# Kernel tuning notes

Measured on AMD Instinct MI355X. Metric: run time of the kernel, lower is better.

## Reference

```python
import jax, jax.numpy as jnp
import numpy as np

N, E, G = 20000, 320000, 64
IN_CH, HID, HEADS = 128, 64, 8
LEAKY_SLOPE = 0.2
SOFTMAX_EPS = 1e-16


def setup_inputs() -> dict:
    key = jax.random.key(0)
    ks = jax.random.split(key, 12)
    s = lambda fan_in: 1.0 / np.sqrt(fan_in)
    return {
        "x": jax.random.normal(ks[0], (N, IN_CH), jnp.float32),
        "edge_index": jax.random.randint(ks[1], (2, E), 0, N, jnp.int32),
        "batch": jnp.sort(jax.random.randint(ks[2], (N,), 0, G, jnp.int32)),
        "W1": jax.random.normal(ks[3], (HEADS * HID, IN_CH), jnp.float32) * s(IN_CH),
        "att_src1": jax.random.normal(ks[4], (HEADS, HID), jnp.float32) * s(HID),
        "att_dst1": jax.random.normal(ks[5], (HEADS, HID), jnp.float32) * s(HID),
        "b1": jnp.zeros((HEADS * HID,), jnp.float32),
        "W2": jax.random.normal(ks[6], (HID, HEADS * HID), jnp.float32) * s(HEADS * HID),
        "att_src2": jax.random.normal(ks[7], (1, HID), jnp.float32) * s(HID),
        "att_dst2": jax.random.normal(ks[8], (1, HID), jnp.float32) * s(HID),
        "b2": jnp.zeros((HID,), jnp.float32),
    }


def gat_conv(x, src, dst, W, att_src, att_dst, b):
    # x: [N, F_in]; W: [H*C, F_in]; att_*: [H, C]; b: [H*C]
    n = x.shape[0]
    heads, ch = att_src.shape
    h = (x @ W.T).reshape(n, heads, ch)                    # [N,H,C]
    a_s = jnp.einsum('nhc,hc->nh', h, att_src)             # [N,H]
    a_d = jnp.einsum('nhc,hc->nh', h, att_dst)             # [N,H]
    e = jax.nn.leaky_relu(a_s[src] + a_d[dst], LEAKY_SLOPE)  # [E,H]
    m = jax.ops.segment_max(e, dst, num_segments=n)        # scatter-softmax (stable)
    e = jnp.exp(e - m[dst])
    z = jax.ops.segment_sum(e, dst, num_segments=n)
    alpha = e / (z[dst] + SOFTMAX_EPS)                     # [E,H]
    msg = h[src] * alpha[:, :, None]                       # [E,H,C]
    out = jax.ops.segment_sum(msg, dst, num_segments=n)    # [N,H,C]
    return out.reshape(n, heads * ch) + b


def reference(x, edge_index, batch, W1, att_src1, att_dst1, b1, W2, att_src2, att_dst2, b2):
    # PyG GATConv default: add self loops
    loop = jnp.arange(N, dtype=edge_index.dtype)
    src = jnp.concatenate([edge_index[0], loop])
    dst = jnp.concatenate([edge_index[1], loop])

    x_mid = jax.nn.relu(gat_conv(x, src, dst, W1, att_src1, att_dst1, b1))  # [N, H*C]

    # global_mean_pool over `batch` segments
    sums = jax.ops.segment_sum(x_mid, batch, num_segments=G)
    cnt = jax.ops.segment_sum(jnp.ones((N,), x_mid.dtype), batch, num_segments=G)
    gat_mid_pooled = sums / jnp.maximum(cnt, 1.0)[:, None]                  # [G, H*C]

    # dropout identity in eval mode
    x_late = gat_conv(x_mid, src, dst, W2, att_src2, att_dst2, b2)          # [N, C]
    gat_late_view = x_late.reshape(-1, HEADS * HID)                          # [N/H, H*C]
    return gat_mid_pooled, gat_late_view
```

## Files before the change

### kernel.cpp

```cpp
#include <hip/hip_runtime.h>
#include <math.h>

#define NN 20000
#define EE 320000
#define ETOT 340000
#define GG 64
#define INCH 128
#define HIDC 64
#define NH 8
#define HC 512
#define SLOPE 0.2f
#define SMEPS 1e-16f

typedef unsigned short u16;
typedef unsigned int u32;
typedef __attribute__((ext_vector_type(8))) short bf16x8;
typedef __attribute__((ext_vector_type(4))) float f32x4;
typedef __attribute__((ext_vector_type(2))) float f32x2;
typedef __attribute__((ext_vector_type(2))) u32 u32x2;

__device__ __forceinline__ float rlanef(float v, int l) {
  return __uint_as_float(__builtin_amdgcn_readlane(__float_as_uint(v), l));
}
__device__ __forceinline__ u16 f2bf(float f) {
  u32 x = __float_as_uint(f);
  x += 0x7FFFu + ((x >> 16) & 1u);
  return (u16)(x >> 16);
}
__device__ __forceinline__ float bflo(u32 w) { return __uint_as_float(w << 16); }
__device__ __forceinline__ float bfhi(u32 w) { return __uint_as_float(w & 0xffff0000u); }

__global__ void k_hist(const int* __restrict__ ei, int* __restrict__ deg) {
  int i = blockIdx.x * 256 + threadIdx.x;
  if (i >= ETOT) return;
  int d = (i < EE) ? ei[EE + i] : (i - EE);
  atomicAdd(&deg[d], 1);
}

__global__ void k_scan(const int* __restrict__ deg, int* __restrict__ rowstart) {
  __shared__ int wsum[16];
  __shared__ int carry_sh;
  int tid = threadIdx.x;
  int lane = tid & 63, w = tid >> 6;
  if (tid == 0) { carry_sh = 0; rowstart[0] = 0; }
  __syncthreads();
  for (int base = 0; base < NN; base += 1024) {
    int v = (base + tid < NN) ? deg[base + tid] : 0;
    int s = v;
#pragma unroll
    for (int off = 1; off < 64; off <<= 1) {
      int t = __shfl_up(s, off);
      if (lane >= off) s += t;
    }
    if (lane == 63) wsum[w] = s;
    __syncthreads();
    if (w == 0 && lane < 16) {
      int t = wsum[lane];
#pragma unroll
      for (int off = 1; off < 16; off <<= 1) {
        int u = __shfl_up(t, off);
        if (lane >= off) t += u;
      }
      wsum[lane] = t;
    }
    __syncthreads();
    int waveoff = (w == 0) ? 0 : wsum[w - 1];
    int incl = s + waveoff + carry_sh;
    if (base + tid < NN) rowstart[base + tid + 1] = incl;
    __syncthreads();
    if (tid == 1023) carry_sh = incl;
    __syncthreads();
  }
}

__global__ void k_fill(const int* __restrict__ ei, const int* __restrict__ rowstart,
                       int* __restrict__ wcur, int* __restrict__ csr) {
  int i = blockIdx.x * 256 + threadIdx.x;
  if (i >= ETOT) return;
  int s, d;
  if (i < EE) { s = ei[i]; d = ei[EE + i]; } else { s = i - EE; d = s; }
  int pos = rowstart[d] + atomicAdd(&wcur[d], 1);
  csr[pos] = s;
}

__global__ void k_prep(const float* __restrict__ W1, const float* __restrict__ W2,
                       const float* __restrict__ as1, const float* __restrict__ ad1v,
                       const float* __restrict__ x,
                       u16* __restrict__ W1bf, u16* __restrict__ W2bf,
                       float* __restrict__ wB1, u16* __restrict__ xbf) {
  int i = blockIdx.x * 256 + threadIdx.x;
  if (i < 65536) {
    W1bf[i] = f2bf(W1[i]);
  } else if (i < 65536 + 32768) {
    int j = i - 65536;
    W2bf[j] = f2bf(W2[j]);
  } else if (i < 65536 + 32768 + 2048) {
    int j = i - 65536 - 32768;
    int k = j >> 4, c = j & 15;
    int h = c & 7;
    const float* av = (c < 8) ? as1 : ad1v;
    float s = 0.f;
    for (int q = 0; q < 64; ++q) s += W1[(h * 64 + q) * 128 + k] * av[h * 64 + q];
    wB1[j] = s;
  } else {
    int j = i - 100352;
    if (j < NN * INCH) xbf[j] = f2bf(x[j]);
  }
}

__global__ __launch_bounds__(256) void k_logits1(
    const float* __restrict__ x, const float* __restrict__ wB1,
    float* __restrict__ al1) {
  __shared__ float bs[128][16];
  int tid = threadIdx.x;
#pragma unroll
  for (int i = 0; i < 8; ++i) {
    int e = tid + i * 256;
    bs[e >> 4][e & 15] = wB1[e];
  }
  __syncthreads();
  int gt = blockIdx.x * 256 + tid;
  int r = gt >> 2; if (r > NN - 1) r = NN - 1;
  int q = gt & 3;
  const float* xp = x + (size_t)r * INCH;
  float acc[4] = {0.f, 0.f, 0.f, 0.f};
  for (int kq = 0; kq < 32; ++kq) {
    float4 a = *(const float4*)(xp + kq * 4);
    float av[4] = {a.x, a.y, a.z, a.w};
#pragma unroll
    for (int kk = 0; kk < 4; ++kk) {
      const float4 b = *(const float4*)&bs[kq * 4 + kk][q * 4];
      acc[0] = fmaf(av[kk], b.x, acc[0]);
      acc[1] = fmaf(av[kk], b.y, acc[1]);
      acc[2] = fmaf(av[kk], b.z, acc[2]);
      acc[3] = fmaf(av[kk], b.w, acc[3]);
    }
  }
  float4 o; o.x = acc[0]; o.y = acc[1]; o.z = acc[2]; o.w = acc[3];
  *(float4*)(al1 + (size_t)r * 16 + q * 4) = o;
}

__global__ __launch_bounds__(256) void k_agg1(
    const u16* __restrict__ xbf, const float* __restrict__ al1,
    const int* __restrict__ rowstart, const int* __restrict__ csr,
    u16* __restrict__ aggbf) {
  int n = blockIdx.x * 4 + (threadIdx.x >> 6);
  int lane = threadIdx.x & 63;
  int rs = __builtin_amdgcn_readfirstlane(rowstart[n]);
  int re = __builtin_amdgcn_readfirstlane(rowstart[n + 1]);
  float4 ad0 = *(const float4*)(al1 + (size_t)n * 16 + 8);
  float4 ad1 = *(const float4*)(al1 + (size_t)n * 16 + 12);
  float zp[NH] = {};
  f32x2 acc2[NH] = {};
  for (int base = rs; base < re; base += 64) {
    int cn = min(64, re - base);
    int idx = base + ((lane < cn) ? lane : 0);
    int s = csr[idx];
    float4 a0 = *(const float4*)(al1 + (size_t)s * 16);
    float4 a1 = *(const float4*)(al1 + (size_t)s * 16 + 4);
    float e[8] = {a0.x + ad0.x, a0.y + ad0.y, a0.z + ad0.z, a0.w + ad0.w,
                  a1.x + ad1.x, a1.y + ad1.y, a1.z + ad1.z, a1.w + ad1.w};
    float p[8];
#pragma unroll
    for (int h = 0; h < 8; ++h) {
      float t = e[h];
      t = fmaxf(t, SLOPE * t);
      float pv = __expf(t);
      pv = (lane < cn) ? pv : 0.f;
      p[h] = pv;
      zp[h] += pv;
    }
    int j = 0;
    for (; j + 1 < cn; j += 2) {
      int sa = __builtin_amdgcn_readlane(s, j);
      int sb = __builtin_amdgcn_readlane(s, j + 1);
      u32 xa = *(const u32*)(xbf + (size_t)sa * INCH + lane * 2);
      u32 xb = *(const u32*)(xbf + (size_t)sb * INCH + lane * 2);
      f32x2 va; va.x = bflo(xa); va.y = bfhi(xa);
      f32x2 vb; vb.x = bflo(xb); vb.y = bfhi(xb);
#pragma unroll
      for (int h = 0; h < 8; ++h) {
        float pa = rlanef(p[h], j);
        float pb = rlanef(p[h], j + 1);
        f32x2 pa2; pa2.x = pa; pa2.y = pa;
        f32x2 pb2; pb2.x = pb; pb2.y = pb;
        acc2[h] = __builtin_elementwise_fma(pa2, va, acc2[h]);
        acc2[h] = __builtin_elementwise_fma(pb2, vb, acc2[h]);
      }
    }
    if (j < cn) {
      int sa = __builtin_amdgcn_readlane(s, j);
      u32 xa = *(const u32*)(xbf + (size_t)sa * INCH + lane * 2);
      f32x2 va; va.x = bflo(xa); va.y = bfhi(xa);
#pragma unroll
      for (int h = 0; h < 8; ++h) {
        float pa = rlanef(p[h], j);
        f32x2 pa2; pa2.x = pa; pa2.y = pa;
        acc2[h] = __builtin_elementwise_fma(pa2, va, acc2[h]);
      }
    }
  }
#pragma unroll
  for (int h = 0; h < 8; ++h) {
    float z = zp[h];
#pragma unroll
    for (int off = 32; off; off >>= 1) z += __shfl_xor(z, off);
    float inv = 1.f / (z + SMEPS);
    u32 pk = ((u32)f2bf(acc2[h].y * inv) << 16) | (u32)f2bf(acc2[h].x * inv);
    *(u32*)(aggbf + (size_t)h * NN * INCH + (size_t)n * INCH + lane * 2) = pk;
  }
}

__global__ __launch_bounds__(256) void k_gemm1h(
    const u16* __restrict__ aggbf, const u16* __restrict__ W1bf,
    const float* __restrict__ b1, u16* __restrict__ xmidbf) {
  int tid = threadIdx.x;
  int head = blockIdx.x & 7;
  int nb = blockIdx.x >> 3;
  int w = tid >> 6, l = tid & 63;
  int li = l & 15, hi = l >> 4;
  const u16* Ab = aggbf + (size_t)head * NN * INCH;
  const u16* Bb = W1bf + (size_t)head * 64 * INCH;

  bf16x8 Bf[4][4];
#pragma unroll
  for (int ks = 0; ks < 4; ++ks)
#pragma unroll
    for (int ct = 0; ct < 4; ++ct)
      Bf[ks][ct] = *(const bf16x8*)(Bb + (size_t)(ct * 16 + li) * INCH + ks * 32 + hi * 8);

  int nA = nb * 64 + w * 16 + li; if (nA > NN - 1) nA = NN - 1;
  const u16* Ap = Ab + (size_t)nA * INCH + hi * 8;
  f32x4 acc[4] = {};
#pragma unroll
  for (int ks = 0; ks < 4; ++ks) {
    bf16x8 Af = *(const bf16x8*)(Ap + ks * 32);
#pragma unroll
    for (int ct = 0; ct < 4; ++ct)
      acc[ct] = __builtin_amdgcn_mfma_f32_16x16x32_bf16(Af, Bf[ks][ct], acc[ct], 0, 0, 0);
  }
#pragma unroll
  for (int ct = 0; ct < 4; ++ct) {
    float bb = b1[head * 64 + ct * 16 + li];
#pragma unroll
    for (int reg = 0; reg < 4; ++reg) {
      int r = nb * 64 + w * 16 + hi * 4 + reg; if (r > NN - 1) r = NN - 1;
      float v = fmaxf(acc[ct][reg] + bb, 0.f);
      xmidbf[(size_t)r * HC + head * 64 + ct * 16 + li] = f2bf(v);
    }
  }
}

__global__ __launch_bounds__(256) void k_gemm2(
    const u16* __restrict__ xmb, const u16* __restrict__ W2bf,
    const float* __restrict__ atts, const float* __restrict__ attd,
    u16* __restrict__ h2bf, float* __restrict__ as2, float* __restrict__ ad2) {
  __shared__ float red[4][16][65];
  int tid = threadIdx.x;
  int w = tid >> 6, l = tid & 63;
  int li = l & 15, hi = l >> 4;
  int brow = blockIdx.x * 16;

  bf16x8 Bf[4][4];
#pragma unroll
  for (int ksl = 0; ksl < 4; ++ksl)
#pragma unroll
    for (int ct = 0; ct < 4; ++ct)
      Bf[ksl][ct] = *(const bf16x8*)(W2bf + (size_t)(ct * 16 + li) * HC + w * 128 + ksl * 32 + hi * 8);

  const u16* Ap = xmb + (size_t)(brow + li) * HC + w * 128 + hi * 8;
  f32x4 acc[4] = {};
#pragma unroll
  for (int ksl = 0; ksl < 4; ++ksl) {
    bf16x8 Af = *(const bf16x8*)(Ap + ksl * 32);
#pragma unroll
    for (int ct = 0; ct < 4; ++ct)
      acc[ct] = __builtin_amdgcn_mfma_f32_16x16x32_bf16(Af, Bf[ksl][ct], acc[ct], 0, 0, 0);
  }
#pragma unroll
  for (int ct = 0; ct < 4; ++ct)
#pragma unroll
    for (int reg = 0; reg < 4; ++reg)
      red[w][hi * 4 + reg][ct * 16 + li] = acc[ct][reg];
  __syncthreads();

  int c = l;
  float atv = atts[c], adv = attd[c];
  float vs[4], vd[4];
#pragma unroll
  for (int i = 0; i < 4; ++i) {
    int r = w + 4 * i;
    float v = red[0][r][c] + red[1][r][c] + red[2][r][c] + red[3][r][c];
    h2bf[(size_t)(brow + r) * HIDC + c] = f2bf(v);
    vs[i] = v * atv; vd[i] = v * adv;
  }
#pragma unroll
  for (int off = 32; off; off >>= 1) {
#pragma unroll
    for (int i = 0; i < 4; ++i) { vs[i] += __shfl_xor(vs[i], off); vd[i] += __shfl_xor(vd[i], off); }
  }
  if (l == 0) {
#pragma unroll
    for (int i = 0; i < 4; ++i) {
      int n = brow + w + 4 * i;
      as2[n] = vs[i]; ad2[n] = vd[i];
    }
  }
}

__global__ __launch_bounds__(256) void k_node2(
    const u16* __restrict__ h2bf, const float* __restrict__ as2, const float* __restrict__ ad2,
    const int* __restrict__ rowstart, const int* __restrict__ csr,
    const float* __restrict__ b2, float* __restrict__ out) {
  int n = blockIdx.x * 4 + (threadIdx.x >> 6);
  int lane = threadIdx.x & 63;
  int e = lane >> 4, c = lane & 15;
  int rs = __builtin_amdgcn_readfirstlane(rowstart[n]);
  int re = __builtin_amdgcn_readfirstlane(rowstart[n + 1]);
  float ad = ad2[n];
  f32x2 accA = {}, accB = {};
  float zp = 0.f;
  for (int base = rs; base < re; base += 4) {
    int idx = base + e;
    bool ok = idx < re;
    int s = csr[ok ? idx : re - 1];
    float t = as2[s] + ad;
    t = fmaxf(t, SLOPE * t);
    float pv = __expf(t);
    float p = ok ? pv : 0.f;
    zp += p;
    const u32* hp = (const u32*)(h2bf + (size_t)s * HIDC + c * 4);
    u32 w0 = hp[0], w1 = hp[1];
    f32x2 v0; v0.x = bflo(w0); v0.y = bfhi(w0);
    f32x2 v1; v1.x = bflo(w1); v1.y = bfhi(w1);
    f32x2 p2; p2.x = p; p2.y = p;
    accA = __builtin_elementwise_fma(p2, v0, accA);
    accB = __builtin_elementwise_fma(p2, v1, accB);
  }
  float acc0 = accA.x, acc1 = accA.y, acc2v = accB.x, acc3 = accB.y;
  zp += __shfl_xor(zp, 16); zp += __shfl_xor(zp, 32);
  acc0 += __shfl_xor(acc0, 16); acc0 += __shfl_xor(acc0, 32);
  acc1 += __shfl_xor(acc1, 16); acc1 += __shfl_xor(acc1, 32);
  acc2v += __shfl_xor(acc2v, 16); acc2v += __shfl_xor(acc2v, 32);
  acc3 += __shfl_xor(acc3, 16); acc3 += __shfl_xor(acc3, 32);
  if (e == 0) {
    float inv = 1.f / (zp + SMEPS);
    float4 bv = *(const float4*)(b2 + c * 4);
    float4 o;
    o.x = acc0 * inv + bv.x; o.y = acc1 * inv + bv.y;
    o.z = acc2v * inv + bv.z; o.w = acc3 * inv + bv.w;
    *(float4*)(out + (size_t)n * HIDC + c * 4) = o;
  }
}

__device__ inline int lowerb(const int* a, int n, int v) {
  int lo = 0, hi = n;
  while (lo < hi) { int mid = (lo + hi) >> 1; if (a[mid] < v) lo = mid + 1; else hi = mid; }
  return lo;
}

__global__ __launch_bounds__(256) void k_pool(const u16* __restrict__ xmb,
                                              const int* __restrict__ batch,
                                              float* __restrict__ out) {
  __shared__ float red[4][128];
  int g = blockIdx.x >> 2;
  int cb = blockIdx.x & 3;
  int tid = threadIdx.x;
  int c2 = tid & 63;
  int rq = tid >> 6;
  int lo = lowerb(batch, NN, g);
  int hi = lowerb(batch, NN, g + 1);
  float sx = 0.f, sy = 0.f;
  for (int n = lo + rq; n < hi; n += 4) {
    u32 w = *(const u32*)(xmb + (size_t)n * HC + cb * 128 + c2 * 2);
    sx += bflo(w); sy += bfhi(w);
  }
  red[rq][c2 * 2] = sx; red[rq][c2 * 2 + 1] = sy;
  __syncthreads();
  if (rq == 0) {
    float inv = 1.f / fmaxf((float)(hi - lo), 1.f);
    float vx = red[0][c2 * 2] + red[1][c2 * 2] + red[2][c2 * 2] + red[3][c2 * 2];
    float vy = red[0][c2 * 2 + 1] + red[1][c2 * 2 + 1] + red[2][c2 * 2 + 1] + red[3][c2 * 2 + 1];
    float2 o; o.x = vx * inv; o.y = vy * inv;
    *(float2*)(out + (size_t)g * HC + cb * 128 + c2 * 2) = o;
  }
}

extern "C" void kernel_launch(void* const* d_in, const int* in_sizes, int n_in,
                              void* d_out, int out_size, void* d_ws, size_t ws_size,
                              hipStream_t stream) {
  const float* x     = (const float*)d_in[0];
  const int*   ei    = (const int*)d_in[1];
  const int*   batch = (const int*)d_in[2];
  const float* W1    = (const float*)d_in[3];
  const float* atts1 = (const float*)d_in[4];
  const float* attd1 = (const float*)d_in[5];
  const float* b1    = (const float*)d_in[6];
  const float* W2    = (const float*)d_in[7];
  const float* atts2 = (const float*)d_in[8];
  const float* attd2 = (const float*)d_in[9];
  const float* b2    = (const float*)d_in[10];
  float* out = (float*)d_out;

  float* ws = (float*)d_ws;
  size_t off = 0;
  u16*  aggbf  = (u16*)(ws + off); off += (size_t)NH * NN * INCH / 2;
  u16*  xmidbf = (u16*)(ws + off); off += (size_t)NN * HC / 2;
  u16*  h2bf   = (u16*)(ws + off); off += (size_t)NN * HIDC / 2;
  float* al1  = ws + off; off += (size_t)NN * 16;
  float* as2  = ws + off; off += NN;
  float* ad2  = ws + off; off += NN;
  u16*  W1bf  = (u16*)(ws + off); off += 65536 / 2;
  u16*  W2bf  = (u16*)(ws + off); off += 32768 / 2;
  float* wB1  = ws + off; off += 2048;
  u16*  xbf   = (u16*)(ws + off); off += (size_t)NN * INCH / 2;
  int* deg      = (int*)(ws + off); off += NN;
  int* wcur     = (int*)(ws + off); off += NN;
  int* rowstart = (int*)(ws + off); off += NN + 4;
  int* csr      = (int*)(ws + off); off += ETOT;

  hipMemsetAsync(deg, 0, sizeof(int) * 2 * NN, stream);
  k_prep<<<10392, 256, 0, stream>>>(W1, W2, atts1, attd1, x, W1bf, W2bf, wB1, xbf);
  k_hist<<<(ETOT + 255) / 256, 256, 0, stream>>>(ei, deg);
  k_scan<<<1, 1024, 0, stream>>>(deg, rowstart);
  k_fill<<<(ETOT + 255) / 256, 256, 0, stream>>>(ei, rowstart, wcur, csr);

  k_logits1<<<313, 256, 0, stream>>>(x, wB1, al1);
  k_agg1<<<5000, 256, 0, stream>>>(xbf, al1, rowstart, csr, aggbf);
  k_gemm1h<<<313 * 8, 256, 0, stream>>>(aggbf, W1bf, b1, xmidbf);
  k_pool<<<GG * 4, 256, 0, stream>>>(xmidbf, batch, out);
  k_gemm2<<<1250, 256, 0, stream>>>(xmidbf, W2bf, atts2, attd2, h2bf, as2, ad2);
  k_node2<<<5000, 256, 0, stream>>>(h2bf, as2, ad2, rowstart, csr, b2, out + (size_t)GG * HC);
}
```

Measured before the change: 200.2 us.

## Fuse histogram into prep, single-pass scan, deeper unroll in aggregation loops

```diff
diff --git a/kernel.cpp b/kernel.cpp
--- a/kernel.cpp
+++ b/kernel.cpp
@@ -17,7 +17,6 @@
 typedef __attribute__((ext_vector_type(8))) short bf16x8;
 typedef __attribute__((ext_vector_type(4))) float f32x4;
 typedef __attribute__((ext_vector_type(2))) float f32x2;
-typedef __attribute__((ext_vector_type(2))) u32 u32x2;
 
 __device__ __forceinline__ float rlanef(float v, int l) {
   return __uint_as_float(__builtin_amdgcn_readlane(__float_as_uint(v), l));
@@ -30,64 +29,22 @@
 __device__ __forceinline__ float bflo(u32 w) { return __uint_as_float(w << 16); }
 __device__ __forceinline__ float bfhi(u32 w) { return __uint_as_float(w & 0xffff0000u); }
 
-__global__ void k_hist(const int* __restrict__ ei, int* __restrict__ deg) {
-  int i = blockIdx.x * 256 + threadIdx.x;
-  if (i >= ETOT) return;
-  int d = (i < EE) ? ei[EE + i] : (i - EE);
-  atomicAdd(&deg[d], 1);
-}
-
-__global__ void k_scan(const int* __restrict__ deg, int* __restrict__ rowstart) {
-  __shared__ int wsum[16];
-  __shared__ int carry_sh;
-  int tid = threadIdx.x;
-  int lane = tid & 63, w = tid >> 6;
-  if (tid == 0) { carry_sh = 0; rowstart[0] = 0; }
-  __syncthreads();
-  for (int base = 0; base < NN; base += 1024) {
-    int v = (base + tid < NN) ? deg[base + tid] : 0;
-    int s = v;
-#pragma unroll
-    for (int off = 1; off < 64; off <<= 1) {
-      int t = __shfl_up(s, off);
-      if (lane >= off) s += t;
-    }
-    if (lane == 63) wsum[w] = s;
-    __syncthreads();
-    if (w == 0 && lane < 16) {
-      int t = wsum[lane];
-#pragma unroll
-      for (int off = 1; off < 16; off <<= 1) {
-        int u = __shfl_up(t, off);
-        if (lane >= off) t += u;
-      }
-      wsum[lane] = t;
-    }
-    __syncthreads();
-    int waveoff = (w == 0) ? 0 : wsum[w - 1];
-    int incl = s + waveoff + carry_sh;
-    if (base + tid < NN) rowstart[base + tid + 1] = incl;
-    __syncthreads();
-    if (tid == 1023) carry_sh = incl;
-    __syncthreads();
-  }
-}
-
-__global__ void k_fill(const int* __restrict__ ei, const int* __restrict__ rowstart,
-                       int* __restrict__ wcur, int* __restrict__ csr) {
-  int i = blockIdx.x * 256 + threadIdx.x;
-  if (i >= ETOT) return;
-  int s, d;
-  if (i < EE) { s = ei[i]; d = ei[EE + i]; } else { s = i - EE; d = s; }
-  int pos = rowstart[d] + atomicAdd(&wcur[d], 1);
-  csr[pos] = s;
-}
-
+#define PREP_B 10392
+#define HIST_B 1329
 __global__ void k_prep(const float* __restrict__ W1, const float* __restrict__ W2,
                        const float* __restrict__ as1, const float* __restrict__ ad1v,
-                       const float* __restrict__ x,
+                       const float* __restrict__ x, const int* __restrict__ ei,
                        u16* __restrict__ W1bf, u16* __restrict__ W2bf,
-                       float* __restrict__ wB1, u16* __restrict__ xbf) {
+                       float* __restrict__ wB1, u16* __restrict__ xbf,
+                       int* __restrict__ deg) {
+  if (blockIdx.x >= PREP_B) {
+    int i = (blockIdx.x - PREP_B) * 256 + threadIdx.x;
+    if (i < ETOT) {
+      int d = (i < EE) ? ei[EE + i] : (i - EE);
+      atomicAdd(&deg[d], 1);
+    }
+    return;
+  }
   int i = blockIdx.x * 256 + threadIdx.x;
   if (i < 65536) {
     W1bf[i] = f2bf(W1[i]);
@@ -106,6 +63,57 @@
     int j = i - 100352;
     if (j < NN * INCH) xbf[j] = f2bf(x[j]);
   }
+}
+
+__global__ __launch_bounds__(1024) void k_scan(const int* __restrict__ deg,
+                                               int* __restrict__ rowstart) {
+  __shared__ int wtot[16];
+  int tid = threadIdx.x;
+  int lane = tid & 63, w = tid >> 6;
+  int base = tid * 20;
+  int v[20];
+  int s = 0;
+#pragma unroll
+  for (int k = 0; k < 20; ++k) {
+    v[k] = (base + k < NN) ? deg[base + k] : 0;
+    s += v[k];
+  }
+  int ps = s;
+#pragma unroll
+  for (int off = 1; off < 64; off <<= 1) {
+    int t = __shfl_up(ps, off);
+    if (lane >= off) ps += t;
+  }
+  if (lane == 63) wtot[w] = ps;
+  __syncthreads();
+  if (w == 0 && lane < 16) {
+    int t = wtot[lane];
+#pragma unroll
+    for (int off = 1; off < 16; off <<= 1) {
+      int u = __shfl_up(t, off);
+      if (lane >= off) t += u;
+    }
+    wtot[lane] = t;
+  }
+  __syncthreads();
+  int woff = (w == 0) ? 0 : wtot[w - 1];
+  int run = woff + ps - s;
+#pragma unroll
+  for (int k = 0; k < 20; ++k) {
+    run += v[k];
+    if (base + k < NN) rowstart[base + k + 1] = run;
+  }
+  if (tid == 0) rowstart[0] = 0;
+}
+
+__global__ void k_fill(const int* __restrict__ ei, const int* __restrict__ rowstart,
+                       int* __restrict__ wcur, int* __restrict__ csr) {
+  int i = blockIdx.x * 256 + threadIdx.x;
+  if (i >= ETOT) return;
+  int s, d;
+  if (i < EE) { s = ei[i]; d = ei[EE + i]; } else { s = i - EE; d = s; }
+  int pos = rowstart[d] + atomicAdd(&wcur[d], 1);
+  csr[pos] = s;
 }
 
 __global__ __launch_bounds__(256) void k_logits1(
@@ -171,24 +179,36 @@
       zp[h] += pv;
     }
     int j = 0;
-    for (; j + 1 < cn; j += 2) {
-      int sa = __builtin_amdgcn_readlane(s, j);
-      int sb = __builtin_amdgcn_readlane(s, j + 1);
-      u32 xa = *(const u32*)(xbf + (size_t)sa * INCH + lane * 2);
-      u32 xb = *(const u32*)(xbf + (size_t)sb * INCH + lane * 2);
-      f32x2 va; va.x = bflo(xa); va.y = bfhi(xa);
-      f32x2 vb; vb.x = bflo(xb); vb.y = bfhi(xb);
+    for (; j + 3 < cn; j += 4) {
+      int s0 = __builtin_amdgcn_readlane(s, j);
+      int s1 = __builtin_amdgcn_readlane(s, j + 1);
+      int s2 = __builtin_amdgcn_readlane(s, j + 2);
+      int s3 = __builtin_amdgcn_readlane(s, j + 3);
+      u32 x0 = *(const u32*)(xbf + (size_t)s0 * INCH + lane * 2);
+      u32 x1 = *(const u32*)(xbf + (size_t)s1 * INCH + lane * 2);
+      u32 x2 = *(const u32*)(xbf + (size_t)s2 * INCH + lane * 2);
+      u32 x3 = *(const u32*)(xbf + (size_t)s3 * INCH + lane * 2);
+      f32x2 v0; v0.x = bflo(x0); v0.y = bfhi(x0);
+      f32x2 v1; v1.x = bflo(x1); v1.y = bfhi(x1);
+      f32x2 v2; v2.x = bflo(x2); v2.y = bfhi(x2);
+      f32x2 v3; v3.x = bflo(x3); v3.y = bfhi(x3);
 #pragma unroll
       for (int h = 0; h < 8; ++h) {
-        float pa = rlanef(p[h], j);
-        float pb = rlanef(p[h], j + 1);
-        f32x2 pa2; pa2.x = pa; pa2.y = pa;
-        f32x2 pb2; pb2.x = pb; pb2.y = pb;
-        acc2[h] = __builtin_elementwise_fma(pa2, va, acc2[h]);
-        acc2[h] = __builtin_elementwise_fma(pb2, vb, acc2[h]);
+        float p0 = rlanef(p[h], j);
+        float p1 = rlanef(p[h], j + 1);
+        float p2 = rlanef(p[h], j + 2);
+        float p3 = rlanef(p[h], j + 3);
+        f32x2 q0; q0.x = p0; q0.y = p0;
+        f32x2 q1; q1.x = p1; q1.y = p1;
+        f32x2 q2; q2.x = p2; q2.y = p2;
+        f32x2 q3; q3.x = p3; q3.y = p3;
+        acc2[h] = __builtin_elementwise_fma(q0, v0, acc2[h]);
+        acc2[h] = __builtin_elementwise_fma(q1, v1, acc2[h]);
+        acc2[h] = __builtin_elementwise_fma(q2, v2, acc2[h]);
+        acc2[h] = __builtin_elementwise_fma(q3, v3, acc2[h]);
       }
     }
-    if (j < cn) {
+    for (; j < cn; ++j) {
       int sa = __builtin_amdgcn_readlane(s, j);
       u32 xa = *(const u32*)(xbf + (size_t)sa * INCH + lane * 2);
       f32x2 va; va.x = bflo(xa); va.y = bfhi(xa);
@@ -320,22 +340,32 @@
   float ad = ad2[n];
   f32x2 accA = {}, accB = {};
   float zp = 0.f;
-  for (int base = rs; base < re; base += 4) {
-    int idx = base + e;
-    bool ok = idx < re;
-    int s = csr[ok ? idx : re - 1];
-    float t = as2[s] + ad;
-    t = fmaxf(t, SLOPE * t);
-    float pv = __expf(t);
-    float p = ok ? pv : 0.f;
-    zp += p;
-    const u32* hp = (const u32*)(h2bf + (size_t)s * HIDC + c * 4);
-    u32 w0 = hp[0], w1 = hp[1];
-    f32x2 v0; v0.x = bflo(w0); v0.y = bfhi(w0);
-    f32x2 v1; v1.x = bflo(w1); v1.y = bfhi(w1);
-    f32x2 p2; p2.x = p; p2.y = p;
-    accA = __builtin_elementwise_fma(p2, v0, accA);
-    accB = __builtin_elementwise_fma(p2, v1, accB);
+  for (int base = rs; base < re; base += 8) {
+    int iA = base + e, iB = base + 4 + e;
+    bool okA = iA < re, okB = iB < re;
+    int sA = csr[okA ? iA : re - 1];
+    int sB = csr[okB ? iB : re - 1];
+    float tA = as2[sA] + ad;
+    float tB = as2[sB] + ad;
+    const u32* hpA = (const u32*)(h2bf + (size_t)sA * HIDC + c * 4);
+    const u32* hpB = (const u32*)(h2bf + (size_t)sB * HIDC + c * 4);
+    u32 a0 = hpA[0], a1 = hpA[1];
+    u32 b0 = hpB[0], b1 = hpB[1];
+    tA = fmaxf(tA, SLOPE * tA);
+    tB = fmaxf(tB, SLOPE * tB);
+    float pA = okA ? __expf(tA) : 0.f;
+    float pB = okB ? __expf(tB) : 0.f;
+    zp += pA + pB;
+    f32x2 vA0; vA0.x = bflo(a0); vA0.y = bfhi(a0);
+    f32x2 vA1; vA1.x = bflo(a1); vA1.y = bfhi(a1);
+    f32x2 vB0; vB0.x = bflo(b0); vB0.y = bfhi(b0);
+    f32x2 vB1; vB1.x = bflo(b1); vB1.y = bfhi(b1);
+    f32x2 pA2; pA2.x = pA; pA2.y = pA;
+    f32x2 pB2; pB2.x = pB; pB2.y = pB;
+    accA = __builtin_elementwise_fma(pA2, vA0, accA);
+    accB = __builtin_elementwise_fma(pA2, vA1, accB);
+    accA = __builtin_elementwise_fma(pB2, vB0, accA);
+    accB = __builtin_elementwise_fma(pB2, vB1, accB);
   }
   float acc0 = accA.x, acc1 = accA.y, acc2v = accB.x, acc3 = accB.y;
   zp += __shfl_xor(zp, 16); zp += __shfl_xor(zp, 32);
@@ -420,8 +450,8 @@
   int* csr      = (int*)(ws + off); off += ETOT;
 
   hipMemsetAsync(deg, 0, sizeof(int) * 2 * NN, stream);
-  k_prep<<<10392, 256, 0, stream>>>(W1, W2, atts1, attd1, x, W1bf, W2bf, wB1, xbf);
-  k_hist<<<(ETOT + 255) / 256, 256, 0, stream>>>(ei, deg);
+  k_prep<<<PREP_B + HIST_B, 256, 0, stream>>>(W1, W2, atts1, attd1, x, ei,
+                                              W1bf, W2bf, wB1, xbf, deg);
   k_scan<<<1, 1024, 0, stream>>>(deg, rowstart);
   k_fill<<<(ETOT + 255) / 256, 256, 0, stream>>>(ei, rowstart, wcur, csr);
 
```

Result: faster. 188.1 us (-6.1%).
